# Performance work log

Hardware: AMD Instinct MI355X
Metric: run time of the kernel (lower is better)

The kernel has to match this reference:

```python
import jax, jax.numpy as jnp
import numpy as np

N_NODES = 100000
N_EDGES = 1600000
N_GRAPHS = 512


def _init_linear(key, fan_in, fan_out):
    kw, kb = jax.random.split(key)
    scale = 1.0 / np.sqrt(fan_in)
    W = jax.random.normal(kw, (fan_in, fan_out), dtype=jnp.float32) * scale
    b = jax.random.normal(kb, (fan_out,), dtype=jnp.float32) * 0.01
    return W, b


def setup_inputs() -> dict:
    key = jax.random.key(0)
    ks = jax.random.split(key, 9)
    x = jax.random.normal(ks[0], (N_NODES, 2), dtype=jnp.float32)
    edge_index = jax.random.randint(ks[1], (2, N_EDGES), 0, N_NODES, dtype=jnp.int64)
    batch = jnp.sort(jax.random.randint(ks[2], (N_NODES,), 0, N_GRAPHS, dtype=jnp.int64))
    dims = [(2, 16), (16, 32), (32, 64), (64, 128), (128, 64), (64, 10)]
    params = {}
    for i, (fi, fo) in enumerate(dims):
        W, b = _init_linear(ks[3 + i], fi, fo)
        params[f"W{i+1}"] = W
        params[f"b{i+1}"] = b
    return dict(x=x, edge_index=edge_index, batch=batch, **params)


def _gcn_layer(x, src, dst, norm, W, b):
    # message = norm * x[src]; aggregate by sum over destination node
    msg = x[src] * norm[:, None]                        # [E+N, C]
    agg = jax.ops.segment_sum(msg, dst, num_segments=N_NODES)  # [N, C]
    return jax.nn.relu(agg @ W + b)


def reference(x, edge_index, batch, W1, b1, W2, b2, W3, b3, W4, b4, W5, b5, W6, b6):
    # GCN with added self-loops and symmetric normalization D^-1/2 A_hat D^-1/2
    self_idx = jnp.arange(N_NODES, dtype=edge_index.dtype)
    src = jnp.concatenate([edge_index[0], self_idx])
    dst = jnp.concatenate([edge_index[1], self_idx])
    deg = jax.ops.segment_sum(jnp.ones_like(dst, dtype=x.dtype), dst, num_segments=N_NODES)
    deg_isqrt = jax.lax.rsqrt(deg)                      # deg >= 1 via self-loops
    norm = deg_isqrt[src] * deg_isqrt[dst]

    h = _gcn_layer(x, src, dst, norm, W1, b1)           # [N, 16]
    h = _gcn_layer(h, src, dst, norm, W2, b2)           # [N, 32]
    h = _gcn_layer(h, src, dst, norm, W3, b3)           # [N, 64]
    h = _gcn_layer(h, src, dst, norm, W4, b4)           # [N, 128]

    # scatter_max graph pooling over batch assignment
    pooled = jax.ops.segment_max(h, batch, num_segments=N_GRAPHS)  # [G, 128]
    pooled = jnp.where(jnp.isfinite(pooled), pooled, 0.0)

    h = jax.nn.relu(pooled @ W5 + b5)                   # [G, 64]
    out = h @ W6 + b6                                   # [G, 10]
    return out
```

## Files before the change

### kernel.cpp

```cpp
#include <hip/hip_runtime.h>
#include <hip/hip_fp16.h>

typedef __attribute__((ext_vector_type(4))) float f32x4;
typedef __attribute__((ext_vector_type(4))) int i32x4;
typedef _Float16 f16x8 __attribute__((ext_vector_type(8)));
typedef _Float16 f16x4 __attribute__((ext_vector_type(4)));

#define EPB 4096
#define NBKT 196
#define BCAP 10240

__global__ __launch_bounds__(256)
void init_kernel(int* __restrict__ bktCur, float* __restrict__ pooled,
                 const float* __restrict__ W, _Float16* __restrict__ Wpk) {
    const int gid = blockIdx.x * 256 + threadIdx.x;
    if (gid < NBKT) bktCur[gid] = 0;
    if (gid < 512 * 128) pooled[gid] = 0.f;
    if (gid < 8192) {
        const int i = gid & 7;
        const int l = (gid >> 3) & 63;
        const int kk = (gid >> 9) & 1;
        const int ct = gid >> 10;
        const int k = kk * 32 + 4 * (l >> 4) + (i & 3) + 16 * (i >> 2);
        const int col = ct * 16 + (l & 15);
        Wpk[gid] = (_Float16)W[k * 128 + col];
    }
}

__global__ __launch_bounds__(256)
void partition_kernel(const int* __restrict__ ei, int E,
                      int* __restrict__ bktCur, int* __restrict__ arena) {
    __shared__ int sHist[256];
    __shared__ int sScan[256];
    __shared__ int sAdj[256];
    __shared__ int2 sEdges[EPB];
    const int t = threadIdx.x;
    const int e0 = blockIdx.x * EPB;
    const int ecnt = min(EPB, E - e0);
    const int* src = ei;
    const int* dst = ei + E;

    sHist[t] = 0;
    __syncthreads();
    for (int k = t; k < ecnt; k += 256) {
        const int s = src[e0 + k], d = dst[e0 + k];
        sEdges[k] = make_int2(s, d);
        atomicAdd(&sHist[d >> 9], 1);
    }
    __syncthreads();
    const int v = sHist[t];
    sScan[t] = v;
    __syncthreads();
    #pragma unroll
    for (int off = 1; off < 256; off <<= 1) {
        const int y = (t >= off) ? sScan[t - off] : 0;
        __syncthreads();
        sScan[t] += y;
        __syncthreads();
    }
    const int excl = sScan[t] - v;
    if (t < NBKT && v > 0) {
        const int g = atomicAdd(&bktCur[t], v);
        sAdj[t] = t * BCAP + g - excl;
    }
    sHist[t] = excl;
    __syncthreads();
    for (int k = t; k < ecnt; k += 256) {
        const int2 e = sEdges[k];
        const int b = e.y >> 9;
        const int p = atomicAdd(&sHist[b], 1);
        arena[sAdj[b] + p] = (e.x << 9) | (e.y & 511);
    }
}

__global__ __launch_bounds__(512)
void bucket_csr_kernel(const int* __restrict__ arena, const int* __restrict__ bktCur,
                       int* __restrict__ csr_src, int2* __restrict__ meta,
                       float* __restrict__ dis, const float* __restrict__ x,
                       float* __restrict__ g0, int n) {
    __shared__ int sHist[512];
    __shared__ int sScan[512];
    const int t = threadIdx.x;
    const int b = blockIdx.x;
    const int base = b * BCAP;
    const int cnt_b = min(bktCur[b], BCAP);

    sHist[t] = 0;
    __syncthreads();
    for (int e = t; e < cnt_b; e += 512)
        atomicAdd(&sHist[arena[base + e] & 511], 1);
    __syncthreads();
    const int v = sHist[t];
    sScan[t] = v;
    __syncthreads();
    #pragma unroll
    for (int off = 1; off < 512; off <<= 1) {
        const int y = (t >= off) ? sScan[t - off] : 0;
        __syncthreads();
        sScan[t] += y;
        __syncthreads();
    }
    const int excl = sScan[t] - v;
    const int node = b * 512 + t;
    if (node < n) {
        meta[node] = make_int2(base + excl, v);
        const float d = (float)(1.0 / sqrt((double)(v + 1)));
        dis[node] = d;
        float2 xv = *(const float2*)(x + 2 * (size_t)node);
        xv.x *= d; xv.y *= d;
        *(float2*)(g0 + 2 * (size_t)node) = xv;
    }
    sHist[t] = excl;
    __syncthreads();
    for (int e = t; e < cnt_b; e += 512) {
        const int pv = arena[base + e];
        const int p = atomicAdd(&sHist[pv & 511], 1);
        csr_src[base + p] = pv >> 9;
    }
}

__global__ __launch_bounds__(256, 4)
void gcn_l1(const float* __restrict__ g0, const int2* __restrict__ meta,
            const int* __restrict__ csr_src, const float* __restrict__ dis,
            const float* __restrict__ W, const float* __restrict__ B,
            __half* __restrict__ g1h, int n, int nwaves) {
    const int lane = threadIdx.x & 63;
    const int wid = blockIdx.x * (blockDim.x >> 6) + (threadIdx.x >> 6);
    const int chunk = (n + nwaves - 1) / nwaves;
    const int n0 = wid * chunk, n1 = min(n0 + chunk, n);
    const int o = lane & 15;
    const float w0 = W[o], w1 = W[16 + o], bo = B[o];
    for (int node = n0; node < n1; ++node) {
        const int2 mt = meta[node];
        const int start = mt.x, m = mt.y;
        float a0 = 0.f, a1 = 0.f;
        for (int j = lane; j < m; j += 64) {
            const int s2 = csr_src[start + j];
            const float2 hv = *(const float2*)(g0 + 2 * (size_t)s2);
            a0 += hv.x;
            a1 += hv.y;
        }
        #pragma unroll
        for (int off = 32; off >= 1; off >>= 1) {
            a0 += __shfl_xor(a0, off);
            a1 += __shfl_xor(a1, off);
        }
        const float d0 = dis[node];
        const float2 hs = *(const float2*)(g0 + 2 * (size_t)node);
        a0 = (a0 + hs.x) * d0;
        a1 = (a1 + hs.y) * d0;
        if (lane < 16) {
            const float v = fmaxf(fmaf(a0, w0, fmaf(a1, w1, bo)), 0.f);
            g1h[(size_t)node * 16 + o] = __float2half(d0 * v);
        }
    }
}

template <int C_IN, bool OUT_HALF>
__global__ __launch_bounds__(256, 6)
void agg_group_kernel(const __half* __restrict__ g_in, const int2* __restrict__ meta,
                      const int* __restrict__ csr_src, const float* __restrict__ dis,
                      void* __restrict__ agg_v, int n) {
    constexpr int LPR = C_IN / 8;
    constexpr int GPW = 64 / LPR;

    const int lane = threadIdx.x & 63;
    const int wv = threadIdx.x >> 6;
    const int grp = lane / LPR;
    const int sl  = lane % LPR;
    const int node = ((size_t)blockIdx.x * 4 + wv) * GPW + grp;
    const bool valid = node < n;

    const int2 mt = valid ? meta[node] : make_int2(0, 0);
    const int start = mt.x, m = mt.y;
    const int cb = sl * 8;

    float a[8];
    #pragma unroll
    for (int q = 0; q < 8; ++q) a[q] = 0.f;

    for (int j = 0; j < m; j += 8) {
        int ss[8];
        float mm[8];
        #pragma unroll
        for (int u = 0; u < 8; ++u) {
            const int jj = j + u;
            const bool ok = jj < m;
            ss[u] = csr_src[start + (ok ? jj : 0)];
            mm[u] = ok ? 1.f : 0.f;
        }
        i32x4 hr[8];
        const __half* ap[8];
        #pragma unroll
        for (int u = 0; u < 8; ++u) ap[u] = g_in + (size_t)ss[u] * C_IN + cb;
        #pragma unroll
        for (int u = 0; u < 8; ++u)
            asm volatile("global_load_dwordx4 %0, %1, off"
                         : "=v"(hr[u]) : "v"(ap[u]) : "memory");
        asm volatile("s_waitcnt vmcnt(0)" ::: "memory");
        __builtin_amdgcn_sched_barrier(0);
        #pragma unroll
        for (int u = 0; u < 8; ++u) {
            #pragma unroll
            for (int q = 0; q < 4; ++q) {
                const int wbits = hr[u][q];
                const __half2 h2 = *(const __half2*)&wbits;
                const float2 f2 = __half22float2(h2);
                a[2 * q]     = fmaf(mm[u], f2.x, a[2 * q]);
                a[2 * q + 1] = fmaf(mm[u], f2.y, a[2 * q + 1]);
            }
        }
    }

    if (valid) {
        const float d0 = dis[node];
        const __half* hp = g_in + (size_t)node * C_IN + cb;
        #pragma unroll
        for (int q = 0; q < 4; ++q) {
            const __half2 h2 = *(const __half2*)(hp + 2 * q);
            const float2 f2 = __half22float2(h2);
            a[2 * q]     = (a[2 * q]     + f2.x) * d0;
            a[2 * q + 1] = (a[2 * q + 1] + f2.y) * d0;
        }
        if constexpr (OUT_HALF) {
            f16x8 t;
            #pragma unroll
            for (int q = 0; q < 8; ++q) t[q] = (_Float16)a[q];
            *(f16x8*)((_Float16*)agg_v + (size_t)node * C_IN + cb) = t;
        } else {
            float* agg = (float*)agg_v;
            f32x4 t0, t1;
            t0.x = a[0]; t0.y = a[1]; t0.z = a[2]; t0.w = a[3];
            t1.x = a[4]; t1.y = a[5]; t1.z = a[6]; t1.w = a[7];
            *(f32x4*)&agg[(size_t)node * C_IN + cb] = t0;
            *(f32x4*)&agg[(size_t)node * C_IN + cb + 4] = t1;
        }
    }
}

template <int C_IN, int C_OUT, bool OUT_HALF>
__global__ __launch_bounds__(256, 3)
void gemm_kernel(const float* __restrict__ agg, const float* __restrict__ W,
                 const float* __restrict__ Bias, const float* __restrict__ dis,
                 void* __restrict__ g_out_v, int n) {
    constexpr int QW = C_OUT / 16;
    constexpr int RPT = QW;
    constexpr int LOGQ = (QW == 8) ? 3 : (QW == 4) ? 2 : 1;
    constexpr int CH = C_IN / 4;
    constexpr int SA = 68;

    constexpr int W_BYTES = C_IN * C_OUT * 4 + C_OUT * 4;
    constexpr int R1 = (W_BYTES + 15) & ~15;
    constexpr int AT_BYTES = C_IN * SA * 4;
    __shared__ char smem[R1 + AT_BYTES];
    __shared__ float sDis[64];

    float* sW = (float*)smem;
    float* sB = sW + C_IN * C_OUT;
    float* sAt = (float*)(smem + R1);

    const int tid = threadIdx.x;
    const int base = blockIdx.x * 64;

    for (int i = tid; i < C_IN * C_OUT / 4; i += 256)
        ((f32x4*)sW)[i] = ((const f32x4*)W)[i];
    if (tid < C_OUT) sB[tid] = Bias[tid];
    {
        constexpr int RPP = 256 / CH;
        const int r = tid / CH, c0 = tid % CH;
        #pragma unroll
        for (int p = 0; p < 64 / RPP; ++p) {
            const int rr = p * RPP + r;
            const int node = base + rr;
            f32x4 v = {0.f, 0.f, 0.f, 0.f};
            if (node < n) v = *(const f32x4*)&agg[(size_t)node * C_IN + c0 * 4];
            sAt[(c0 * 4 + 0) * SA + rr] = v.x;
            sAt[(c0 * 4 + 1) * SA + rr] = v.y;
            sAt[(c0 * 4 + 2) * SA + rr] = v.z;
            sAt[(c0 * 4 + 3) * SA + rr] = v.w;
        }
    }
    if (tid < 64) sDis[tid] = (base + tid < n) ? dis[base + tid] : 0.f;
    __syncthreads();

    const int w = tid >> 6, l = tid & 63;
    const int j = l & (QW - 1);
    const int rg = l >> LOGQ;
    const int ob = w * (C_OUT / 4) + j * 4;

    f32x4 acc[RPT];
    {
        const f32x4 bv = *(const f32x4*)&sB[ob];
        #pragma unroll
        for (int r = 0; r < RPT; ++r) acc[r] = bv;
    }

    #pragma unroll 4
    for (int k = 0; k < C_IN; ++k) {
        const f32x4 wv = ((const f32x4*)sW)[k * (C_OUT / 4) + (ob >> 2)];
        float av[RPT];
        if constexpr (RPT == 4) {
            const f32x4 a0 = *(const f32x4*)&sAt[k * SA + rg * 4];
            av[0] = a0.x; av[1] = a0.y; av[2] = a0.z; av[3] = a0.w;
        } else {
            const float2 a0 = *(const float2*)&sAt[k * SA + rg * 2];
            av[0] = a0.x; av[1] = a0.y;
        }
        #pragma unroll
        for (int r = 0; r < RPT; ++r) {
            acc[r].x = fmaf(av[r], wv.x, acc[r].x);
            acc[r].y = fmaf(av[r], wv.y, acc[r].y);
            acc[r].z = fmaf(av[r], wv.z, acc[r].z);
            acc[r].w = fmaf(av[r], wv.w, acc[r].w);
        }
    }

    #pragma unroll
    for (int r = 0; r < RPT; ++r) {
        const int row = rg * RPT + r;
        const int node = base + row;
        if (node < n) {
            const float sd = sDis[row];
            const float o0 = sd * fmaxf(acc[r].x, 0.f);
            const float o1 = sd * fmaxf(acc[r].y, 0.f);
            const float o2 = sd * fmaxf(acc[r].z, 0.f);
            const float o3 = sd * fmaxf(acc[r].w, 0.f);
            if constexpr (OUT_HALF) {
                __half2 lo = __floats2half2_rn(o0, o1);
                __half2 hi = __floats2half2_rn(o2, o3);
                uint2 pk;
                pk.x = *(unsigned int*)&lo;
                pk.y = *(unsigned int*)&hi;
                *(uint2*)((__half*)g_out_v + (size_t)node * C_OUT + ob) = pk;
            } else {
                f32x4 o; o.x = o0; o.y = o1; o.z = o2; o.w = o3;
                *(f32x4*)((float*)g_out_v + (size_t)node * C_OUT + ob) = o;
            }
        }
    }
}

__global__ __launch_bounds__(256)
void gemm4_mfma_kernel(const _Float16* __restrict__ aggh, const _Float16* __restrict__ Wpk,
                       const float* __restrict__ Bias, const int* __restrict__ batchv,
                       float* __restrict__ pooled, int n) {
    __shared__ float sP[4][16][132];
    __shared__ int sGb[64];

    const int tid = threadIdx.x;
    const int w = tid >> 6, l = tid & 63;
    const int base = blockIdx.x * 64;

    if (tid < 64) sGb[tid] = (base + tid < n) ? batchv[base + tid] : -1;

    int node_a = base + w * 16 + (l & 15);
    if (node_a >= n) node_a = n - 1;
    const int kb = l >> 4;
    const f16x4* rowp = (const f16x4*)(aggh + (size_t)node_a * 64);
    const f16x4 a00 = rowp[kb];
    const f16x4 a01 = rowp[4 + kb];
    const f16x4 a10 = rowp[8 + kb];
    const f16x4 a11 = rowp[12 + kb];
    const f16x8 a0 = __builtin_shufflevector(a00, a01, 0, 1, 2, 3, 4, 5, 6, 7);
    const f16x8 a1 = __builtin_shufflevector(a10, a11, 0, 1, 2, 3, 4, 5, 6, 7);

    f32x4 acc[8];
    #pragma unroll
    for (int ct = 0; ct < 8; ++ct) {
        f32x4 z = {0.f, 0.f, 0.f, 0.f};
        const f16x8 b0 = *(const f16x8*)(Wpk + ((ct * 2 + 0) * 64 + l) * 8);
        const f16x8 b1 = *(const f16x8*)(Wpk + ((ct * 2 + 1) * 64 + l) * 8);
        z = __builtin_amdgcn_mfma_f32_16x16x32_f16(a0, b0, z, 0, 0, 0);
        z = __builtin_amdgcn_mfma_f32_16x16x32_f16(a1, b1, z, 0, 0, 0);
        acc[ct] = z;
    }

    #pragma unroll
    for (int ct = 0; ct < 8; ++ct) {
        const float b = Bias[ct * 16 + (l & 15)];
        #pragma unroll
        for (int r = 0; r < 4; ++r) {
            const int m = (l >> 4) * 4 + r;
            sP[w][m][ct * 16 + (l & 15)] = fmaxf(acc[ct][r] + b, 0.f);
        }
    }
    __syncthreads();

    if (tid < 128) {
        const int c = tid;
        int curg = -1; float run = 0.f;
        for (int r2 = 0; r2 < 64; ++r2) {
            const int gb = sGb[r2];
            if (gb < 0) continue;
            const float v = sP[r2 >> 4][r2 & 15][c];
            if (gb != curg) {
                if (curg >= 0)
                    atomicMax((int*)&pooled[(size_t)curg * 128 + c], __float_as_int(run));
                curg = gb; run = v;
            } else {
                run = fmaxf(run, v);
            }
        }
        if (curg >= 0)
            atomicMax((int*)&pooled[(size_t)curg * 128 + c], __float_as_int(run));
    }
}

__global__ void mlp_kernel(const float* __restrict__ pooled,
                           const float* __restrict__ W5, const float* __restrict__ b5,
                           const float* __restrict__ W6, const float* __restrict__ b6,
                           float* __restrict__ out) {
    const int g = blockIdx.x;
    const int t = threadIdx.x;
    __shared__ float row[128];
    __shared__ float hid[64];
    row[t] = pooled[g * 128 + t];
    row[64 + t] = pooled[g * 128 + 64 + t];
    __syncthreads();
    float v = b5[t];
    #pragma unroll 8
    for (int c = 0; c < 128; ++c) v = fmaf(row[c], W5[c * 64 + t], v);
    hid[t] = fmaxf(v, 0.f);
    __syncthreads();
    if (t < 10) {
        float o = b6[t];
        #pragma unroll 8
        for (int c = 0; c < 64; ++c) o = fmaf(hid[c], W6[c * 10 + t], o);
        out[g * 10 + t] = o;
    }
}

extern "C" void kernel_launch(void* const* d_in, const int* in_sizes, int n_in,
                              void* d_out, int out_size, void* d_ws, size_t ws_size,
                              hipStream_t stream) {
    const float* x     = (const float*)d_in[0];
    const int*   ei    = (const int*)d_in[1];
    const int*   batch = (const int*)d_in[2];
    const float* W1 = (const float*)d_in[3];  const float* b1 = (const float*)d_in[4];
    const float* W2 = (const float*)d_in[5];  const float* b2 = (const float*)d_in[6];
    const float* W3 = (const float*)d_in[7];  const float* b3 = (const float*)d_in[8];
    const float* W4 = (const float*)d_in[9];  const float* b4 = (const float*)d_in[10];
    const float* W5 = (const float*)d_in[11]; const float* b5 = (const float*)d_in[12];
    const float* W6 = (const float*)d_in[13]; const float* b6 = (const float*)d_in[14];
    float* out = (float*)d_out;

    const int N = in_sizes[0] / 2;
    const int E = in_sizes[1] / 2;
    const int G = out_size / 10;

    char* p = (char*)d_ws;
    auto take = [&](size_t bytes) -> void* {
        void* r = (void*)p;
        p += (bytes + 255) & ~(size_t)255;
        return r;
    };
    int*       bktCur = (int*)take(NBKT * 4);
    int*       arena  = (int*)take((size_t)NBKT * BCAP * 4);
    int*       csr_src= (int*)take((size_t)NBKT * BCAP * 4);
    float*     dis    = (float*)take((size_t)N * 4);
    int2*      meta   = (int2*)take((size_t)N * 8);
    float*     g0     = (float*)take((size_t)N * 2 * 4);
    __half*    g1h    = (__half*)take((size_t)N * 16 * 2);
    __half*    g2h    = (__half*)take((size_t)N * 32 * 2);
    __half*    g3h    = (__half*)take((size_t)N * 64 * 2);
    float*     aggb   = (float*)take((size_t)N * 32 * 4);
    _Float16*  aggh   = (_Float16*)take((size_t)N * 64 * 2);
    _Float16*  Wpk    = (_Float16*)take(8192 * 2);
    float*     pooled = (float*)take((size_t)G * 128 * 4);

    init_kernel<<<(512 * 128 + 255) / 256, 256, 0, stream>>>(bktCur, pooled, W4, Wpk);

    const int PBLK = (E + EPB - 1) / EPB;
    partition_kernel<<<PBLK, 256, 0, stream>>>(ei, E, bktCur, arena);
    bucket_csr_kernel<<<NBKT, 512, 0, stream>>>(arena, bktCur, csr_src, meta, dis, x, g0, N);

    gcn_l1<<<2048, 256, 0, stream>>>(g0, meta, csr_src, dis, W1, b1, g1h, N, 2048 * 4);

    const int GBLK = (N + 63) / 64;

    agg_group_kernel<16, false><<<(N + 127) / 128, 256, 0, stream>>>(g1h, meta, csr_src, dis, aggb, N);
    gemm_kernel<16, 32, true><<<GBLK, 256, 0, stream>>>(aggb, W2, b2, dis, g2h, N);

    agg_group_kernel<32, false><<<(N + 63) / 64, 256, 0, stream>>>(g2h, meta, csr_src, dis, aggb, N);
    gemm_kernel<32, 64, true><<<GBLK, 256, 0, stream>>>(aggb, W3, b3, dis, g3h, N);

    agg_group_kernel<64, true><<<(N + 31) / 32, 256, 0, stream>>>(g3h, meta, csr_src, dis, aggh, N);
    gemm4_mfma_kernel<<<GBLK, 256, 0, stream>>>(aggh, Wpk, b4, batch, pooled, N);

    mlp_kernel<<<G, 64, 0, stream>>>(pooled, W5, b5, W6, b6, out);
}
```

Baseline: 187.8 us.

## Fuse aggregation with dense transform for layers 3 and 4, thread-per-node layer 1

Layers 3 and 4 now each run as one kernel: it gathers neighbor features into shared memory, then applies the dense weight transform. For layer 4 that transform also feeds the MFMA path and the max-pooling. This removes the global round-trips of the intermediate aggregate buffers and two kernel launches. Layer 1 changes from one wave per node with a shuffle reduction to one thread per node with batched gather loads. The cost is more shared memory per block and lower occupancy in the fused kernels.

```diff
diff --git a/kernel.cpp b/kernel.cpp
--- a/kernel.cpp
+++ b/kernel.cpp
@@ -2,6 +2,7 @@
 #include <hip/hip_fp16.h>
 
 typedef __attribute__((ext_vector_type(4))) float f32x4;
+typedef __attribute__((ext_vector_type(2))) float f32x2;
 typedef __attribute__((ext_vector_type(4))) int i32x4;
 typedef _Float16 f16x8 __attribute__((ext_vector_type(8)));
 typedef _Float16 f16x4 __attribute__((ext_vector_type(4)));
@@ -119,41 +120,61 @@
     }
 }
 
-__global__ __launch_bounds__(256, 4)
-void gcn_l1(const float* __restrict__ g0, const int2* __restrict__ meta,
-            const int* __restrict__ csr_src, const float* __restrict__ dis,
-            const float* __restrict__ W, const float* __restrict__ B,
-            __half* __restrict__ g1h, int n, int nwaves) {
-    const int lane = threadIdx.x & 63;
-    const int wid = blockIdx.x * (blockDim.x >> 6) + (threadIdx.x >> 6);
-    const int chunk = (n + nwaves - 1) / nwaves;
-    const int n0 = wid * chunk, n1 = min(n0 + chunk, n);
-    const int o = lane & 15;
-    const float w0 = W[o], w1 = W[16 + o], bo = B[o];
-    for (int node = n0; node < n1; ++node) {
-        const int2 mt = meta[node];
-        const int start = mt.x, m = mt.y;
-        float a0 = 0.f, a1 = 0.f;
-        for (int j = lane; j < m; j += 64) {
-            const int s2 = csr_src[start + j];
-            const float2 hv = *(const float2*)(g0 + 2 * (size_t)s2);
-            a0 += hv.x;
-            a1 += hv.y;
-        }
-        #pragma unroll
-        for (int off = 32; off >= 1; off >>= 1) {
-            a0 += __shfl_xor(a0, off);
-            a1 += __shfl_xor(a1, off);
-        }
-        const float d0 = dis[node];
-        const float2 hs = *(const float2*)(g0 + 2 * (size_t)node);
-        a0 = (a0 + hs.x) * d0;
-        a1 = (a1 + hs.y) * d0;
-        if (lane < 16) {
-            const float v = fmaxf(fmaf(a0, w0, fmaf(a1, w1, bo)), 0.f);
-            g1h[(size_t)node * 16 + o] = __float2half(d0 * v);
-        }
-    }
+__global__ __launch_bounds__(256, 6)
+void gcn_l1_lane(const float* __restrict__ g0, const int2* __restrict__ meta,
+                 const int* __restrict__ csr_src, const float* __restrict__ dis,
+                 const float* __restrict__ W, const float* __restrict__ B,
+                 __half* __restrict__ g1h, int n) {
+    __shared__ float sW[32];
+    __shared__ float sB[16];
+    const int tid = threadIdx.x;
+    if (tid < 32) sW[tid] = W[tid];
+    if (tid < 16) sB[tid] = B[tid];
+    __syncthreads();
+    const int node = blockIdx.x * 256 + tid;
+    if (node >= n) return;
+    const int2 mt = meta[node];
+    const int start = mt.x, m = mt.y;
+    float a0 = 0.f, a1 = 0.f;
+    for (int j = 0; j < m; j += 8) {
+        int ss[8]; float mm[8];
+        #pragma unroll
+        for (int u = 0; u < 8; ++u) {
+            const int jj = j + u;
+            const bool ok = jj < m;
+            ss[u] = csr_src[start + (ok ? jj : 0)];
+            mm[u] = ok ? 1.f : 0.f;
+        }
+        f32x2 hv[8];
+        const float* ap[8];
+        #pragma unroll
+        for (int u = 0; u < 8; ++u) ap[u] = g0 + 2 * (size_t)ss[u];
+        #pragma unroll
+        for (int u = 0; u < 8; ++u)
+            asm volatile("global_load_dwordx2 %0, %1, off"
+                         : "=v"(hv[u]) : "v"(ap[u]) : "memory");
+        asm volatile("s_waitcnt vmcnt(0)" ::: "memory");
+        __builtin_amdgcn_sched_barrier(0);
+        #pragma unroll
+        for (int u = 0; u < 8; ++u) {
+            a0 = fmaf(mm[u], hv[u].x, a0);
+            a1 = fmaf(mm[u], hv[u].y, a1);
+        }
+    }
+    const float d0 = dis[node];
+    const float2 hs = *(const float2*)(g0 + 2 * (size_t)node);
+    a0 = (a0 + hs.x) * d0;
+    a1 = (a1 + hs.y) * d0;
+    f16x8 o0, o1;
+    #pragma unroll
+    for (int o = 0; o < 8; ++o) {
+        const float v0 = fmaxf(fmaf(a0, sW[o], fmaf(a1, sW[16 + o], sB[o])), 0.f);
+        const float v1 = fmaxf(fmaf(a0, sW[o + 8], fmaf(a1, sW[24 + o], sB[o + 8])), 0.f);
+        o0[o] = (_Float16)(d0 * v0);
+        o1[o] = (_Float16)(d0 * v1);
+    }
+    *(f16x8*)((_Float16*)g1h + (size_t)node * 16) = o0;
+    *(f16x8*)((_Float16*)g1h + (size_t)node * 16 + 8) = o1;
 }
 
 template <int C_IN, bool OUT_HALF>
@@ -180,8 +201,7 @@
     for (int q = 0; q < 8; ++q) a[q] = 0.f;
 
     for (int j = 0; j < m; j += 8) {
-        int ss[8];
-        float mm[8];
+        int ss[8]; float mm[8];
         #pragma unroll
         for (int u = 0; u < 8; ++u) {
             const int jj = j + u;
@@ -340,36 +360,230 @@
     }
 }
 
-__global__ __launch_bounds__(256)
-void gemm4_mfma_kernel(const _Float16* __restrict__ aggh, const _Float16* __restrict__ Wpk,
-                       const float* __restrict__ Bias, const int* __restrict__ batchv,
-                       float* __restrict__ pooled, int n) {
-    __shared__ float sP[4][16][132];
+__global__ __launch_bounds__(256, 6)
+void fused_layer3(const __half* __restrict__ g2h, const int2* __restrict__ meta,
+                  const int* __restrict__ csr_src, const float* __restrict__ dis,
+                  const float* __restrict__ W, const float* __restrict__ Bias,
+                  __half* __restrict__ g3h, int n) {
+    constexpr int SA = 68;
+    __shared__ float sW[32 * 64];
+    __shared__ float sB[64];
+    __shared__ float sAt[32 * SA];
+    __shared__ float sDis[64];
+
+    const int tid = threadIdx.x;
+    const int base = blockIdx.x * 64;
+    const int lane = tid & 63, wv = tid >> 6;
+
+    for (int i = tid; i < 32 * 64 / 4; i += 256)
+        ((f32x4*)sW)[i] = ((const f32x4*)W)[i];
+    if (tid < 64) sB[tid] = Bias[tid];
+    if (tid < 64) sDis[tid] = (base + tid < n) ? dis[base + tid] : 0.f;
+
+    {
+        const int row = wv * 16 + (lane >> 2);
+        const int sl = lane & 3;
+        const int cb = sl * 8;
+        const int node = base + row;
+        const bool valid = node < n;
+        const int2 mt = valid ? meta[node] : make_int2(0, 0);
+        const int start = mt.x, m = mt.y;
+
+        float a[8];
+        #pragma unroll
+        for (int q = 0; q < 8; ++q) a[q] = 0.f;
+
+        for (int j = 0; j < m; j += 8) {
+            int ss[8]; float mm[8];
+            #pragma unroll
+            for (int u = 0; u < 8; ++u) {
+                const int jj = j + u;
+                const bool ok = jj < m;
+                ss[u] = csr_src[start + (ok ? jj : 0)];
+                mm[u] = ok ? 1.f : 0.f;
+            }
+            i32x4 hr[8];
+            const __half* ap[8];
+            #pragma unroll
+            for (int u = 0; u < 8; ++u) ap[u] = g2h + (size_t)ss[u] * 32 + cb;
+            #pragma unroll
+            for (int u = 0; u < 8; ++u)
+                asm volatile("global_load_dwordx4 %0, %1, off"
+                             : "=v"(hr[u]) : "v"(ap[u]) : "memory");
+            asm volatile("s_waitcnt vmcnt(0)" ::: "memory");
+            __builtin_amdgcn_sched_barrier(0);
+            #pragma unroll
+            for (int u = 0; u < 8; ++u) {
+                #pragma unroll
+                for (int q = 0; q < 4; ++q) {
+                    const int wbits = hr[u][q];
+                    const __half2 h2 = *(const __half2*)&wbits;
+                    const float2 f2 = __half22float2(h2);
+                    a[2 * q]     = fmaf(mm[u], f2.x, a[2 * q]);
+                    a[2 * q + 1] = fmaf(mm[u], f2.y, a[2 * q + 1]);
+                }
+            }
+        }
+        float d0 = 0.f;
+        if (valid) {
+            d0 = dis[node];
+            const __half* hp = g2h + (size_t)node * 32 + cb;
+            #pragma unroll
+            for (int q = 0; q < 4; ++q) {
+                const __half2 h2 = *(const __half2*)(hp + 2 * q);
+                const float2 f2 = __half22float2(h2);
+                a[2 * q]     = (a[2 * q]     + f2.x) * d0;
+                a[2 * q + 1] = (a[2 * q + 1] + f2.y) * d0;
+            }
+        }
+        #pragma unroll
+        for (int q = 0; q < 8; ++q)
+            sAt[(cb + q) * SA + row] = valid ? a[q] : 0.f;
+    }
+    __syncthreads();
+
+    const int j = lane & 3;
+    const int rg = lane >> 2;
+    const int ob = wv * 16 + j * 4;
+
+    f32x4 acc[4];
+    {
+        const f32x4 bv = *(const f32x4*)&sB[ob];
+        #pragma unroll
+        for (int r = 0; r < 4; ++r) acc[r] = bv;
+    }
+    #pragma unroll 4
+    for (int k = 0; k < 32; ++k) {
+        const f32x4 wvv = ((const f32x4*)sW)[k * 16 + (ob >> 2)];
+        const f32x4 a0 = *(const f32x4*)&sAt[k * SA + rg * 4];
+        float av[4] = {a0.x, a0.y, a0.z, a0.w};
+        #pragma unroll
+        for (int r = 0; r < 4; ++r) {
+            acc[r].x = fmaf(av[r], wvv.x, acc[r].x);
+            acc[r].y = fmaf(av[r], wvv.y, acc[r].y);
+            acc[r].z = fmaf(av[r], wvv.z, acc[r].z);
+            acc[r].w = fmaf(av[r], wvv.w, acc[r].w);
+        }
+    }
+    #pragma unroll
+    for (int r = 0; r < 4; ++r) {
+        const int row = rg * 4 + r;
+        const int node = base + row;
+        if (node < n) {
+            const float sd = sDis[row];
+            __half2 lo = __floats2half2_rn(sd * fmaxf(acc[r].x, 0.f), sd * fmaxf(acc[r].y, 0.f));
+            __half2 hi = __floats2half2_rn(sd * fmaxf(acc[r].z, 0.f), sd * fmaxf(acc[r].w, 0.f));
+            uint2 pk;
+            pk.x = *(unsigned int*)&lo;
+            pk.y = *(unsigned int*)&hi;
+            *(uint2*)((__half*)g3h + (size_t)node * 64 + ob) = pk;
+        }
+    }
+}
+
+__global__ __launch_bounds__(256, 4)
+void fused_layer4(const __half* __restrict__ g3h, const int2* __restrict__ meta,
+                  const int* __restrict__ csr_src, const float* __restrict__ dis,
+                  const _Float16* __restrict__ Wpk, const float* __restrict__ Bias,
+                  const int* __restrict__ batchv, float* __restrict__ pooled, int n) {
+    constexpr int SA = 68;
+    constexpr int AT_BYTES = 64 * SA * 4;
+    constexpr int P_BYTES = 4 * 16 * 132 * 4;
+    __shared__ char smem[(AT_BYTES > P_BYTES ? AT_BYTES : P_BYTES)];
     __shared__ int sGb[64];
+    float* sAt = (float*)smem;
+    float* sP = (float*)smem;
 
     const int tid = threadIdx.x;
-    const int w = tid >> 6, l = tid & 63;
+    const int lane = tid & 63, wv = tid >> 6;
     const int base = blockIdx.x * 64;
 
     if (tid < 64) sGb[tid] = (base + tid < n) ? batchv[base + tid] : -1;
 
-    int node_a = base + w * 16 + (l & 15);
-    if (node_a >= n) node_a = n - 1;
-    const int kb = l >> 4;
-    const f16x4* rowp = (const f16x4*)(aggh + (size_t)node_a * 64);
-    const f16x4 a00 = rowp[kb];
-    const f16x4 a01 = rowp[4 + kb];
-    const f16x4 a10 = rowp[8 + kb];
-    const f16x4 a11 = rowp[12 + kb];
-    const f16x8 a0 = __builtin_shufflevector(a00, a01, 0, 1, 2, 3, 4, 5, 6, 7);
-    const f16x8 a1 = __builtin_shufflevector(a10, a11, 0, 1, 2, 3, 4, 5, 6, 7);
+    {
+        const int grp = wv * 8 + (lane >> 3);
+        const int sl = lane & 7;
+        const int cb = sl * 8;
+        #pragma unroll 1
+        for (int rr = 0; rr < 2; ++rr) {
+            const int row = grp + rr * 32;
+            const int node = base + row;
+            const bool valid = node < n;
+            const int2 mt = valid ? meta[node] : make_int2(0, 0);
+            const int start = mt.x, m = mt.y;
+
+            float a[8];
+            #pragma unroll
+            for (int q = 0; q < 8; ++q) a[q] = 0.f;
+
+            for (int j = 0; j < m; j += 8) {
+                int ss[8]; float mm[8];
+                #pragma unroll
+                for (int u = 0; u < 8; ++u) {
+                    const int jj = j + u;
+                    const bool ok = jj < m;
+                    ss[u] = csr_src[start + (ok ? jj : 0)];
+                    mm[u] = ok ? 1.f : 0.f;
+                }
+                i32x4 hr[8];
+                const __half* ap[8];
+                #pragma unroll
+                for (int u = 0; u < 8; ++u) ap[u] = g3h + (size_t)ss[u] * 64 + cb;
+                #pragma unroll
+                for (int u = 0; u < 8; ++u)
+                    asm volatile("global_load_dwordx4 %0, %1, off"
+                                 : "=v"(hr[u]) : "v"(ap[u]) : "memory");
+                asm volatile("s_waitcnt vmcnt(0)" ::: "memory");
+                __builtin_amdgcn_sched_barrier(0);
+                #pragma unroll
+                for (int u = 0; u < 8; ++u) {
+                    #pragma unroll
+                    for (int q = 0; q < 4; ++q) {
+                        const int wbits = hr[u][q];
+                        const __half2 h2 = *(const __half2*)&wbits;
+                        const float2 f2 = __half22float2(h2);
+                        a[2 * q]     = fmaf(mm[u], f2.x, a[2 * q]);
+                        a[2 * q + 1] = fmaf(mm[u], f2.y, a[2 * q + 1]);
+                    }
+                }
+            }
+            float d0 = 0.f;
+            if (valid) {
+                d0 = dis[node];
+                const __half* hp = g3h + (size_t)node * 64 + cb;
+                #pragma unroll
+                for (int q = 0; q < 4; ++q) {
+                    const __half2 h2 = *(const __half2*)(hp + 2 * q);
+                    const float2 f2 = __half22float2(h2);
+                    a[2 * q]     = (a[2 * q]     + f2.x) * d0;
+                    a[2 * q + 1] = (a[2 * q + 1] + f2.y) * d0;
+                }
+            }
+            #pragma unroll
+            for (int q = 0; q < 8; ++q)
+                sAt[(cb + q) * SA + row] = valid ? a[q] : 0.f;
+        }
+    }
+    __syncthreads();
+
+    const int row_a = wv * 16 + (lane & 15);
+    const int kb = lane >> 4;
+    f16x8 a0, a1;
+    #pragma unroll
+    for (int i = 0; i < 8; ++i) {
+        const int k0 = 4 * kb + (i & 3) + 16 * (i >> 2);
+        const int k1 = 32 + k0;
+        a0[i] = (_Float16)sAt[k0 * SA + row_a];
+        a1[i] = (_Float16)sAt[k1 * SA + row_a];
+    }
+    __syncthreads();
 
     f32x4 acc[8];
     #pragma unroll
     for (int ct = 0; ct < 8; ++ct) {
         f32x4 z = {0.f, 0.f, 0.f, 0.f};
-        const f16x8 b0 = *(const f16x8*)(Wpk + ((ct * 2 + 0) * 64 + l) * 8);
-        const f16x8 b1 = *(const f16x8*)(Wpk + ((ct * 2 + 1) * 64 + l) * 8);
+        const f16x8 b0 = *(const f16x8*)(Wpk + ((ct * 2 + 0) * 64 + lane) * 8);
+        const f16x8 b1 = *(const f16x8*)(Wpk + ((ct * 2 + 1) * 64 + lane) * 8);
         z = __builtin_amdgcn_mfma_f32_16x16x32_f16(a0, b0, z, 0, 0, 0);
         z = __builtin_amdgcn_mfma_f32_16x16x32_f16(a1, b1, z, 0, 0, 0);
         acc[ct] = z;
@@ -377,11 +591,11 @@
 
     #pragma unroll
     for (int ct = 0; ct < 8; ++ct) {
-        const float b = Bias[ct * 16 + (l & 15)];
+        const float b = Bias[ct * 16 + (lane & 15)];
         #pragma unroll
         for (int r = 0; r < 4; ++r) {
-            const int m = (l >> 4) * 4 + r;
-            sP[w][m][ct * 16 + (l & 15)] = fmaxf(acc[ct][r] + b, 0.f);
+            const int mrow = (lane >> 4) * 4 + r;
+            sP[(wv * 16 + mrow) * 132 + ct * 16 + (lane & 15)] = fmaxf(acc[ct][r] + b, 0.f);
         }
     }
     __syncthreads();
@@ -392,7 +606,7 @@
         for (int r2 = 0; r2 < 64; ++r2) {
             const int gb = sGb[r2];
             if (gb < 0) continue;
-            const float v = sP[r2 >> 4][r2 & 15][c];
+            const float v = sP[r2 * 132 + c];
             if (gb != curg) {
                 if (curg >= 0)
                     atomicMax((int*)&pooled[(size_t)curg * 128 + c], __float_as_int(run));
@@ -463,8 +677,7 @@
     __half*    g1h    = (__half*)take((size_t)N * 16 * 2);
     __half*    g2h    = (__half*)take((size_t)N * 32 * 2);
     __half*    g3h    = (__half*)take((size_t)N * 64 * 2);
-    float*     aggb   = (float*)take((size_t)N * 32 * 4);
-    _Float16*  aggh   = (_Float16*)take((size_t)N * 64 * 2);
+    float*     aggb   = (float*)take((size_t)N * 16 * 4);
     _Float16*  Wpk    = (_Float16*)take(8192 * 2);
     float*     pooled = (float*)take((size_t)G * 128 * 4);
 
@@ -474,18 +687,15 @@
     partition_kernel<<<PBLK, 256, 0, stream>>>(ei, E, bktCur, arena);
     bucket_csr_kernel<<<NBKT, 512, 0, stream>>>(arena, bktCur, csr_src, meta, dis, x, g0, N);
 
-    gcn_l1<<<2048, 256, 0, stream>>>(g0, meta, csr_src, dis, W1, b1, g1h, N, 2048 * 4);
+    gcn_l1_lane<<<(N + 255) / 256, 256, 0, stream>>>(g0, meta, csr_src, dis, W1, b1, g1h, N);
 
     const int GBLK = (N + 63) / 64;
 
     agg_group_kernel<16, false><<<(N + 127) / 128, 256, 0, stream>>>(g1h, meta, csr_src, dis, aggb, N);
     gemm_kernel<16, 32, true><<<GBLK, 256, 0, stream>>>(aggb, W2, b2, dis, g2h, N);
 
-    agg_group_kernel<32, false><<<(N + 63) / 64, 256, 0, stream>>>(g2h, meta, csr_src, dis, aggb, N);
-    gemm_kernel<32, 64, true><<<GBLK, 256, 0, stream>>>(aggb, W3, b3, dis, g3h, N);
-
-    agg_group_kernel<64, true><<<(N + 31) / 32, 256, 0, stream>>>(g3h, meta, csr_src, dis, aggh, N);
-    gemm4_mfma_kernel<<<GBLK, 256, 0, stream>>>(aggh, Wpk, b4, batch, pooled, N);
+    fused_layer3<<<GBLK, 256, 0, stream>>>(g2h, meta, csr_src, dis, W3, b3, g3h, N);
+    fused_layer4<<<GBLK, 256, 0, stream>>>(g3h, meta, csr_src, dis, Wpk, b4, batch, pooled, N);
 
     mlp_kernel<<<G, 64, 0, stream>>>(pooled, W5, b5, W6, b6, out);
 }
```

New measurement: 169.7 us. -9.6%, faster.
